# Kernel tuning notes

Measured on AMD Instinct MI355X. Metric: run time of the kernel, lower is better.

## Reference

```python
import jax, jax.numpy as jnp
import numpy as np

EPS = 1e-06


def _feature_map(x):
    # elu(x) + 1  (elu with alpha=1)
    return jnp.where(x > 0, x + 1.0, jnp.exp(x))


def setup_inputs() -> dict:
    key = jax.random.key(0)
    k1, k2, k3 = jax.random.split(key, 3)
    N, L, S, H, D = 4, 8192, 8192, 8, 64
    q = jax.random.normal(k1, (N, L, H, D), dtype=jnp.float32)
    k = jax.random.normal(k2, (N, S, H, D), dtype=jnp.float32)
    v = jax.random.normal(k3, (N, S, H, D), dtype=jnp.float32)
    q_mask = jnp.ones((N, L), dtype=jnp.float32)
    kv_mask = jnp.ones((N, S), dtype=jnp.float32)
    return {"q": q, "k": k, "v": v, "q_mask": q_mask, "kv_mask": kv_mask}


def reference(q, k, v, q_mask, kv_mask):
    # Linear attention with elu+1 feature map (Katharopoulos et al.)
    qf = _feature_map(q)  # [N, L, H, D]
    kf = _feature_map(k)  # [N, S, H, D]
    qf = q_mask[:, :, None, None] * qf
    kf = kv_mask[:, :, None, None] * kf
    vm = kv_mask[:, :, None, None] * v
    S = v.shape[1]
    # global KV state: [N, H, D, Dv]; v scaled by 1/S for numerical stability
    kv = jnp.einsum('nshd,nshv->nhdv', kf, vm / S)
    # normalizer: einsum('nlhd,nshd->nlh') == q . sum_s(k)
    k_sum = kf.sum(axis=1)  # [N, H, D]
    div = 1.0 / (jnp.einsum('nlhd,nhd->nlh', qf, k_sum) + EPS)
    out = S * jnp.einsum('nlhd,nhdv,nlh->nlhv', qf, kv, div)
    return out
```

## Files before the change

kernel.cpp:

```cpp
#include <hip/hip_runtime.h>
#include <math.h>


#define EPS 1e-6f

static constexpr int Nc = 4;
static constexpr int Lc = 8192;
static constexpr int Sc = 8192;
static constexpr int Hc = 8;
static constexpr int NH = Nc * Hc;
static constexpr int STATE = 64 * 64 + 64;
static constexpr int TS = 32;
static constexpr int TSP = 36;
static constexpr int QSP = 68;

typedef __attribute__((ext_vector_type(4))) short short4v;
typedef __attribute__((ext_vector_type(8))) short short8v;
typedef __attribute__((ext_vector_type(4))) float f32x4;

__device__ __forceinline__ float fmap(float x) {
    return x > 0.f ? x + 1.f : __expf(x);
}
__device__ __forceinline__ unsigned short f2bf(float x) {
    unsigned int u = __float_as_uint(x);
    u += 0x7FFFu + ((u >> 16) & 1u);
    return (unsigned short)(u >> 16);
}
__device__ __forceinline__ float bf2f(unsigned short h) {
    return __uint_as_float(((unsigned int)h) << 16);
}
__device__ __forceinline__ short8v ld8(const unsigned short* p) {
    short4v a = *(const short4v*)p;
    short4v b = *(const short4v*)(p + 4);
    return __builtin_shufflevector(a, b, 0, 1, 2, 3, 4, 5, 6, 7);
}
__device__ __forceinline__ unsigned int pack2(unsigned short a, unsigned short b) {
    return (unsigned)a | ((unsigned)b << 16);
}

__global__ __launch_bounds__(256, 4) void k1_partial(
    const float* __restrict__ kg, const float* __restrict__ vg,
    const float* __restrict__ kv_mask,
    float* __restrict__ partial, int chunks, int sc)
{
    __shared__ unsigned short kTh[64][TSP], kTl[64][TSP];
    __shared__ unsigned short vTh[64][TSP], vTl[64][TSP];
    __shared__ float ksb[16][64];

    const int bid = blockIdx.x;
    const int pair = bid / chunks;
    const int chunk = bid - pair * chunks;
    const int n = pair >> 3;
    const int h = pair & 7;
    const int s0 = chunk * sc;
    const int t = threadIdx.x;
    const int g = t >> 4;
    const int c4 = (t & 15) * 4;
    const int lane = t & 63;
    const int wv = t >> 6;
    const int row16 = lane & 15;
    const int g8 = (lane >> 4) * 8;

    f32x4 acc[4] = {{0.f,0.f,0.f,0.f},{0.f,0.f,0.f,0.f},
                    {0.f,0.f,0.f,0.f},{0.f,0.f,0.f,0.f}};
    float ksm[4] = {0.f, 0.f, 0.f, 0.f};

    const size_t rowstride = (size_t)Hc * 64;
    const size_t gbase = ((size_t)n * Sc * Hc + h) * 64 + c4;
    const int mbase = n * Sc;

    float4 kp0, kp1, vp0, vp1;
    float mpe, mpo;

    {
        const int s = s0 + 2 * g;
        const size_t be = gbase + (size_t)s * rowstride;
        kp0 = *(const float4*)(kg + be);
        kp1 = *(const float4*)(kg + be + rowstride);
        vp0 = *(const float4*)(vg + be);
        vp1 = *(const float4*)(vg + be + rowstride);
        mpe = kv_mask[mbase + s];
        mpo = kv_mask[mbase + s + 1];
    }

    for (int sb = 0; sb < sc; sb += TS) {
        const float4 ck0 = kp0, ck1 = kp1, cv0 = vp0, cv1 = vp1;
        const float cme = mpe, cmo = mpo;

        {
            const int nxt = (sb + TS < sc) ? sb + TS : sb;
            const int s = s0 + nxt + 2 * g;
            const size_t be = gbase + (size_t)s * rowstride;
            kp0 = *(const float4*)(kg + be);
            kp1 = *(const float4*)(kg + be + rowstride);
            vp0 = *(const float4*)(vg + be);
            vp1 = *(const float4*)(vg + be + rowstride);
            mpe = kv_mask[mbase + s];
            mpo = kv_mask[mbase + s + 1];
        }

        const float* kep = &ck0.x;
        const float* kop = &ck1.x;
        const float* vep = &cv0.x;
        const float* vop = &cv1.x;
        #pragma unroll
        for (int j = 0; j < 4; ++j) {
            const float fe = cme * fmap(kep[j]);
            const float fo = cmo * fmap(kop[j]);
            ksm[j] += fe + fo;
            const unsigned short he = f2bf(fe), ho = f2bf(fo);
            const unsigned short le = f2bf(fe - bf2f(he)), lo_ = f2bf(fo - bf2f(ho));
            *(unsigned int*)&kTh[c4 + j][2 * g] = pack2(he, ho);
            *(unsigned int*)&kTl[c4 + j][2 * g] = pack2(le, lo_);
            const float ue = cme * vep[j];
            const float uo = cmo * vop[j];
            const unsigned short vhe = f2bf(ue), vho = f2bf(uo);
            const unsigned short vle = f2bf(ue - bf2f(vhe)), vlo = f2bf(uo - bf2f(vho));
            *(unsigned int*)&vTh[c4 + j][2 * g] = pack2(vhe, vho);
            *(unsigned int*)&vTl[c4 + j][2 * g] = pack2(vle, vlo);
        }
        __syncthreads();

        const short8v Ah = ld8(&kTh[wv * 16 + row16][g8]);
        const short8v Al = ld8(&kTl[wv * 16 + row16][g8]);
        #pragma unroll
        for (int bt = 0; bt < 4; ++bt) {
            const short8v Bh = ld8(&vTh[bt * 16 + row16][g8]);
            const short8v Bl = ld8(&vTl[bt * 16 + row16][g8]);
            acc[bt] = __builtin_amdgcn_mfma_f32_16x16x32_bf16(Ah, Bh, acc[bt], 0, 0, 0);
            acc[bt] = __builtin_amdgcn_mfma_f32_16x16x32_bf16(Al, Bh, acc[bt], 0, 0, 0);
            acc[bt] = __builtin_amdgcn_mfma_f32_16x16x32_bf16(Ah, Bl, acc[bt], 0, 0, 0);
        }
        __syncthreads();
    }

    float* outp = partial + (size_t)bid * STATE;
    #pragma unroll
    for (int bt = 0; bt < 4; ++bt) {
        #pragma unroll
        for (int r = 0; r < 4; ++r) {
            outp[(size_t)(wv * 16 + (lane >> 4) * 4 + r) * 64 + bt * 16 + (lane & 15)]
                = acc[bt][r];
        }
    }

    *(f32x4*)&ksb[g][c4] = (f32x4){ksm[0], ksm[1], ksm[2], ksm[3]};
    __syncthreads();
    if (t < 64) {
        float s = 0.f;
        #pragma unroll
        for (int i = 0; i < 16; ++i) s += ksb[i][t];
        outp[4096 + t] = s;
    }
}

__global__ __launch_bounds__(256) void k2_reduce(
    const float* __restrict__ src, float* __restrict__ dst, int nred)
{
    const int p = blockIdx.x / 5;
    const int seg = blockIdx.x - p * 5;
    const int e4 = seg * 256 + threadIdx.x;
    if (e4 >= STATE / 4) return;
    const float4* s = (const float4*)(src + (size_t)p * nred * STATE) + e4;
    float4 acc = make_float4(0.f, 0.f, 0.f, 0.f);
    #pragma unroll 4
    for (int j = 0; j < nred; ++j) {
        float4 x = s[(size_t)j * (STATE / 4)];
        acc.x += x.x; acc.y += x.y; acc.z += x.z; acc.w += x.w;
    }
    ((float4*)(dst + (size_t)p * STATE))[e4] = acc;
}

__global__ __launch_bounds__(256) void k2b_finalize(
    const float* __restrict__ src, float* __restrict__ dst, int nred)
{
    __shared__ float kv[64][QSP];
    __shared__ float kss[64];

    const int pair = blockIdx.x;
    const int t = threadIdx.x;
    const float4* sbase = (const float4*)(src + (size_t)pair * nred * STATE);

    #pragma unroll
    for (int i = 0; i < 4; ++i) {
        const int e4 = t + i * 256;
        float4 a = make_float4(0.f, 0.f, 0.f, 0.f);
        for (int j = 0; j < nred; ++j) {
            float4 x = sbase[(size_t)j * (STATE / 4) + e4];
            a.x += x.x; a.y += x.y; a.z += x.z; a.w += x.w;
        }
        *(float4*)&kv[e4 >> 4][(e4 & 15) * 4] = a;
    }
    if (t < 16) {
        float4 a = make_float4(0.f, 0.f, 0.f, 0.f);
        for (int j = 0; j < nred; ++j) {
            float4 x = sbase[(size_t)j * (STATE / 4) + 1024 + t];
            a.x += x.x; a.y += x.y; a.z += x.z; a.w += x.w;
        }
        *(float4*)&kss[t * 4] = a;
    }
    __syncthreads();

    unsigned int* dw = (unsigned int*)(dst + (size_t)pair * STATE);
    #pragma unroll
    for (int i = 0; i < 8; ++i) {
        const int w = t + i * 256;
        const int dv = w >> 5;
        const int d0 = (w & 31) * 2;
        const float f0 = kv[d0][dv];
        const float f1 = kv[d0 + 1][dv];
        const unsigned short h0 = f2bf(f0), h1 = f2bf(f1);
        dw[w] = pack2(h0, h1);
        dw[2048 + w] = pack2(f2bf(f0 - bf2f(h0)), f2bf(f1 - bf2f(h1)));
    }
    if (t < 64) dst[(size_t)pair * STATE + 4096 + t] = kss[t];
}

__global__ __launch_bounds__(256, 4) void k3_out(
    const float* __restrict__ qg, const float* __restrict__ state,
    const float* __restrict__ q_mask, float* __restrict__ outg)
{
    __shared__ __align__(16) unsigned short qsp[2][64][QSP];
    __shared__ unsigned short kvt[2][64][QSP];
    __shared__ float ksum[64];
    __shared__ float dinv[64];

    const int nblk = Lc / 64;
    const int bid = blockIdx.x;
    const int pair = bid / nblk;
    const int lblk = bid - pair * nblk;
    const int n = pair >> 3;
    const int h = pair & 7;
    const int l0 = lblk * 64;
    const int t = threadIdx.x;
    const int lane = t & 63;
    const int wv = t >> 6;
    const int row16 = lane & 15;
    const int g8 = (lane >> 4) * 8;

    const unsigned int* sw = (const unsigned int*)(state + (size_t)pair * STATE);
    #pragma unroll
    for (int i = 0; i < 8; ++i) {
        const int w = t + i * 256;
        const int dv = w >> 5;
        const int d2 = (w & 31) * 2;
        *(unsigned int*)&kvt[0][dv][d2] = sw[w];
        *(unsigned int*)&kvt[1][dv][d2] = sw[2048 + w];
    }
    if (t < 64) ksum[t] = ((const float*)state)[(size_t)pair * STATE + 4096 + t];
    __syncthreads();

    #pragma unroll
    for (int p = 0; p < 4; ++p) {
        const int f = t + p * 256;
        const int row = f >> 4;
        const int c4 = (f & 15) * 4;
        const int l = l0 + row;
        const size_t base = ((size_t)(n * Lc + l) * Hc + h) * 64 + c4;
        const float4 qq = *(const float4*)(qg + base);
        const float m = q_mask[n * Lc + l];
        const float q0 = m * fmap(qq.x), q1 = m * fmap(qq.y);
        const float q2 = m * fmap(qq.z), q3 = m * fmap(qq.w);
        const unsigned short h0 = f2bf(q0), h1 = f2bf(q1), h2 = f2bf(q2), h3 = f2bf(q3);
        *(unsigned int*)&qsp[0][row][c4]     = pack2(h0, h1);
        *(unsigned int*)&qsp[0][row][c4 + 2] = pack2(h2, h3);
        *(unsigned int*)&qsp[1][row][c4]     = pack2(f2bf(q0 - bf2f(h0)), f2bf(q1 - bf2f(h1)));
        *(unsigned int*)&qsp[1][row][c4 + 2] = pack2(f2bf(q2 - bf2f(h2)), f2bf(q3 - bf2f(h3)));
        float dp = q0 * ksum[c4] + q1 * ksum[c4 + 1] + q2 * ksum[c4 + 2] + q3 * ksum[c4 + 3];
        dp += __shfl_xor(dp, 1);
        dp += __shfl_xor(dp, 2);
        dp += __shfl_xor(dp, 4);
        dp += __shfl_xor(dp, 8);
        if ((t & 15) == 0) dinv[row] = 1.0f / (dp + EPS);
    }
    __syncthreads();

    f32x4 acc[4] = {{0.f,0.f,0.f,0.f},{0.f,0.f,0.f,0.f},
                    {0.f,0.f,0.f,0.f},{0.f,0.f,0.f,0.f}};
    #pragma unroll
    for (int ks = 0; ks < 2; ++ks) {
        const short8v Ah = ld8(&qsp[0][wv * 16 + row16][ks * 32 + g8]);
        const short8v Al = ld8(&qsp[1][wv * 16 + row16][ks * 32 + g8]);
        #pragma unroll
        for (int bt = 0; bt < 4; ++bt) {
            const short8v Bh = ld8(&kvt[0][bt * 16 + row16][ks * 32 + g8]);
            const short8v Bl = ld8(&kvt[1][bt * 16 + row16][ks * 32 + g8]);
            acc[bt] = __builtin_amdgcn_mfma_f32_16x16x32_bf16(Ah, Bh, acc[bt], 0, 0, 0);
            acc[bt] = __builtin_amdgcn_mfma_f32_16x16x32_bf16(Al, Bh, acc[bt], 0, 0, 0);
            acc[bt] = __builtin_amdgcn_mfma_f32_16x16x32_bf16(Ah, Bl, acc[bt], 0, 0, 0);
        }
    }
    __syncthreads();

    float (*outs)[QSP] = reinterpret_cast<float (*)[QSP]>(&qsp[0][0][0]);
    #pragma unroll
    for (int bt = 0; bt < 4; ++bt) {
        #pragma unroll
        for (int r = 0; r < 4; ++r) {
            const int row = wv * 16 + (lane >> 4) * 4 + r;
            outs[row][bt * 16 + row16] = acc[bt][r] * dinv[row];
        }
    }
    __syncthreads();

    #pragma unroll
    for (int p = 0; p < 4; ++p) {
        const int f = t + p * 256;
        const int row = f >> 4;
        const int c4 = (f & 15) * 4;
        const size_t base = ((size_t)(n * Lc + l0 + row) * Hc + h) * 64 + c4;
        *(float4*)(outg + base) = *(const float4*)&outs[row][c4];
    }
}

extern "C" void kernel_launch(void* const* d_in, const int* in_sizes, int n_in,
                              void* d_out, int out_size, void* d_ws, size_t ws_size,
                              hipStream_t stream)
{
    (void)in_sizes; (void)n_in; (void)out_size;
    const float* q       = (const float*)d_in[0];
    const float* k       = (const float*)d_in[1];
    const float* v       = (const float*)d_in[2];
    const float* q_mask  = (const float*)d_in[3];
    const float* kv_mask = (const float*)d_in[4];
    float* out = (float*)d_out;

    const size_t stBytes  = (size_t)STATE * sizeof(float);
    const size_t finBytes = (size_t)NH * stBytes;
    const size_t p2Bytes  = (size_t)NH * 4 * stBytes;

    float* fin = (float*)d_ws;
    float* p2  = (float*)((char*)d_ws + finBytes);
    float* p1  = (float*)((char*)d_ws + finBytes + p2Bytes);

    int chunks = 0;
    for (int c = 64; c >= 8; c >>= 1) {
        if (ws_size >= finBytes + p2Bytes + (size_t)NH * c * stBytes) { chunks = c; break; }
    }

    if (chunks >= 8) {
        k1_partial<<<NH * chunks, 256, 0, stream>>>(k, v, kv_mask, p1, chunks, Sc / chunks);
        k2_reduce<<<NH * 4 * 5, 256, 0, stream>>>(p1, p2, chunks / 4);
        k2b_finalize<<<NH, 256, 0, stream>>>(p2, fin, 4);
    } else {
        float* p1fb = (float*)((char*)d_ws + finBytes);
        k1_partial<<<NH, 256, 0, stream>>>(k, v, kv_mask, p1fb, 1, Sc);
        k2b_finalize<<<NH, 256, 0, stream>>>(p1fb, fin, 1);
    }

    k3_out<<<NH * (Lc / 64), 256, 0, stream>>>(q, fin, q_mask, out);
}
```

Before: 84.81 us.

## Restructure KV-state kernel to single-wave blocks without barriers

The partial KV-state kernel now runs one 64-thread wavefront per block instead of four waves. That single wave loads and converts the whole 32-row tile itself and computes all 16 output tiles of the 64x64 state. This removes the __syncthreads barriers and the shared-memory reduction of the k-sum, which now uses warp shuffles. In exchange, the register-based prefetch of the next tile is dropped, each block has four times as many accumulators and four times the load work, and fewer threads are resident per block. Latency hiding now depends on having many blocks resident at once.

```diff
diff --git a/kernel.cpp b/kernel.cpp
--- a/kernel.cpp
+++ b/kernel.cpp
@@ -38,14 +38,13 @@
     return (unsigned)a | ((unsigned)b << 16);
 }
 
-__global__ __launch_bounds__(256, 4) void k1_partial(
+__global__ __launch_bounds__(64, 2) void k1_partial(
     const float* __restrict__ kg, const float* __restrict__ vg,
     const float* __restrict__ kv_mask,
     float* __restrict__ partial, int chunks, int sc)
 {
     __shared__ unsigned short kTh[64][TSP], kTl[64][TSP];
     __shared__ unsigned short vTh[64][TSP], vTl[64][TSP];
-    __shared__ float ksb[16][64];
 
     const int bid = blockIdx.x;
     const int pair = bid / chunks;
@@ -53,104 +52,88 @@
     const int n = pair >> 3;
     const int h = pair & 7;
     const int s0 = chunk * sc;
-    const int t = threadIdx.x;
-    const int g = t >> 4;
-    const int c4 = (t & 15) * 4;
-    const int lane = t & 63;
-    const int wv = t >> 6;
-    const int row16 = lane & 15;
-    const int g8 = (lane >> 4) * 8;
-
-    f32x4 acc[4] = {{0.f,0.f,0.f,0.f},{0.f,0.f,0.f,0.f},
-                    {0.f,0.f,0.f,0.f},{0.f,0.f,0.f,0.f}};
+    const int l = threadIdx.x;
+    const int row16 = l & 15;
+    const int lg = l >> 4;
+    const int c4 = row16 * 4;
+    const int g8 = lg * 8;
+
+    f32x4 acc[4][4] = {};
     float ksm[4] = {0.f, 0.f, 0.f, 0.f};
 
     const size_t rowstride = (size_t)Hc * 64;
     const size_t gbase = ((size_t)n * Sc * Hc + h) * 64 + c4;
     const int mbase = n * Sc;
 
-    float4 kp0, kp1, vp0, vp1;
-    float mpe, mpo;
-
-    {
-        const int s = s0 + 2 * g;
-        const size_t be = gbase + (size_t)s * rowstride;
-        kp0 = *(const float4*)(kg + be);
-        kp1 = *(const float4*)(kg + be + rowstride);
-        vp0 = *(const float4*)(vg + be);
-        vp1 = *(const float4*)(vg + be + rowstride);
-        mpe = kv_mask[mbase + s];
-        mpo = kv_mask[mbase + s + 1];
-    }
-
     for (int sb = 0; sb < sc; sb += TS) {
-        const float4 ck0 = kp0, ck1 = kp1, cv0 = vp0, cv1 = vp1;
-        const float cme = mpe, cmo = mpo;
-
-        {
-            const int nxt = (sb + TS < sc) ? sb + TS : sb;
-            const int s = s0 + nxt + 2 * g;
+        #pragma unroll
+        for (int jj = 0; jj < 4; ++jj) {
+            const int r0 = jj * 8 + lg * 2;
+            const int s = s0 + sb + r0;
             const size_t be = gbase + (size_t)s * rowstride;
-            kp0 = *(const float4*)(kg + be);
-            kp1 = *(const float4*)(kg + be + rowstride);
-            vp0 = *(const float4*)(vg + be);
-            vp1 = *(const float4*)(vg + be + rowstride);
-            mpe = kv_mask[mbase + s];
-            mpo = kv_mask[mbase + s + 1];
-        }
-
-        const float* kep = &ck0.x;
-        const float* kop = &ck1.x;
-        const float* vep = &cv0.x;
-        const float* vop = &cv1.x;
-        #pragma unroll
-        for (int j = 0; j < 4; ++j) {
-            const float fe = cme * fmap(kep[j]);
-            const float fo = cmo * fmap(kop[j]);
-            ksm[j] += fe + fo;
-            const unsigned short he = f2bf(fe), ho = f2bf(fo);
-            const unsigned short le = f2bf(fe - bf2f(he)), lo_ = f2bf(fo - bf2f(ho));
-            *(unsigned int*)&kTh[c4 + j][2 * g] = pack2(he, ho);
-            *(unsigned int*)&kTl[c4 + j][2 * g] = pack2(le, lo_);
-            const float ue = cme * vep[j];
-            const float uo = cmo * vop[j];
-            const unsigned short vhe = f2bf(ue), vho = f2bf(uo);
-            const unsigned short vle = f2bf(ue - bf2f(vhe)), vlo = f2bf(uo - bf2f(vho));
-            *(unsigned int*)&vTh[c4 + j][2 * g] = pack2(vhe, vho);
-            *(unsigned int*)&vTl[c4 + j][2 * g] = pack2(vle, vlo);
-        }
-        __syncthreads();
-
-        const short8v Ah = ld8(&kTh[wv * 16 + row16][g8]);
-        const short8v Al = ld8(&kTl[wv * 16 + row16][g8]);
+            const float4 k0 = *(const float4*)(kg + be);
+            const float4 k1 = *(const float4*)(kg + be + rowstride);
+            const float4 v0 = *(const float4*)(vg + be);
+            const float4 v1 = *(const float4*)(vg + be + rowstride);
+            const float m0 = kv_mask[mbase + s];
+            const float m1 = kv_mask[mbase + s + 1];
+            const float* ke = &k0.x;
+            const float* ko = &k1.x;
+            const float* ve = &v0.x;
+            const float* vo = &v1.x;
+            #pragma unroll
+            for (int j = 0; j < 4; ++j) {
+                const float fe = m0 * fmap(ke[j]);
+                const float fo = m1 * fmap(ko[j]);
+                ksm[j] += fe + fo;
+                const unsigned short he = f2bf(fe), ho = f2bf(fo);
+                *(unsigned int*)&kTh[c4 + j][r0] = pack2(he, ho);
+                *(unsigned int*)&kTl[c4 + j][r0] =
+                    pack2(f2bf(fe - bf2f(he)), f2bf(fo - bf2f(ho)));
+                const float ue = m0 * ve[j];
+                const float uo = m1 * vo[j];
+                const unsigned short vhe = f2bf(ue), vho = f2bf(uo);
+                *(unsigned int*)&vTh[c4 + j][r0] = pack2(vhe, vho);
+                *(unsigned int*)&vTl[c4 + j][r0] =
+                    pack2(f2bf(ue - bf2f(vhe)), f2bf(uo - bf2f(vho)));
+            }
+        }
+
+        short8v Ah[4], Al[4];
+        #pragma unroll
+        for (int dt = 0; dt < 4; ++dt) {
+            Ah[dt] = ld8(&kTh[dt * 16 + row16][g8]);
+            Al[dt] = ld8(&kTl[dt * 16 + row16][g8]);
+        }
         #pragma unroll
         for (int bt = 0; bt < 4; ++bt) {
             const short8v Bh = ld8(&vTh[bt * 16 + row16][g8]);
             const short8v Bl = ld8(&vTl[bt * 16 + row16][g8]);
-            acc[bt] = __builtin_amdgcn_mfma_f32_16x16x32_bf16(Ah, Bh, acc[bt], 0, 0, 0);
-            acc[bt] = __builtin_amdgcn_mfma_f32_16x16x32_bf16(Al, Bh, acc[bt], 0, 0, 0);
-            acc[bt] = __builtin_amdgcn_mfma_f32_16x16x32_bf16(Ah, Bl, acc[bt], 0, 0, 0);
-        }
-        __syncthreads();
+            #pragma unroll
+            for (int dt = 0; dt < 4; ++dt) {
+                acc[dt][bt] = __builtin_amdgcn_mfma_f32_16x16x32_bf16(Ah[dt], Bh, acc[dt][bt], 0, 0, 0);
+                acc[dt][bt] = __builtin_amdgcn_mfma_f32_16x16x32_bf16(Al[dt], Bh, acc[dt][bt], 0, 0, 0);
+                acc[dt][bt] = __builtin_amdgcn_mfma_f32_16x16x32_bf16(Ah[dt], Bl, acc[dt][bt], 0, 0, 0);
+            }
+        }
     }
 
     float* outp = partial + (size_t)bid * STATE;
     #pragma unroll
-    for (int bt = 0; bt < 4; ++bt) {
-        #pragma unroll
-        for (int r = 0; r < 4; ++r) {
-            outp[(size_t)(wv * 16 + (lane >> 4) * 4 + r) * 64 + bt * 16 + (lane & 15)]
-                = acc[bt][r];
-        }
-    }
-
-    *(f32x4*)&ksb[g][c4] = (f32x4){ksm[0], ksm[1], ksm[2], ksm[3]};
-    __syncthreads();
-    if (t < 64) {
-        float s = 0.f;
-        #pragma unroll
-        for (int i = 0; i < 16; ++i) s += ksb[i][t];
-        outp[4096 + t] = s;
+    for (int dt = 0; dt < 4; ++dt)
+        #pragma unroll
+        for (int bt = 0; bt < 4; ++bt)
+            #pragma unroll
+            for (int r = 0; r < 4; ++r)
+                outp[(size_t)(dt * 16 + lg * 4 + r) * 64 + bt * 16 + row16]
+                    = acc[dt][bt][r];
+
+    #pragma unroll
+    for (int j = 0; j < 4; ++j) {
+        float s = ksm[j];
+        s += __shfl_xor(s, 16);
+        s += __shfl_xor(s, 32);
+        if (lg == 0) outp[4096 + c4 + j] = s;
     }
 }
 
@@ -339,12 +322,12 @@
     }
 
     if (chunks >= 8) {
-        k1_partial<<<NH * chunks, 256, 0, stream>>>(k, v, kv_mask, p1, chunks, Sc / chunks);
+        k1_partial<<<NH * chunks, 64, 0, stream>>>(k, v, kv_mask, p1, chunks, Sc / chunks);
         k2_reduce<<<NH * 4 * 5, 256, 0, stream>>>(p1, p2, chunks / 4);
         k2b_finalize<<<NH, 256, 0, stream>>>(p2, fin, 4);
     } else {
         float* p1fb = (float*)((char*)d_ws + finBytes);
-        k1_partial<<<NH, 256, 0, stream>>>(k, v, kv_mask, p1fb, 1, Sc);
+        k1_partial<<<NH, 64, 0, stream>>>(k, v, kv_mask, p1fb, 1, Sc);
         k2b_finalize<<<NH, 256, 0, stream>>>(p1fb, fin, 1);
     }
 
```

New measurement: 85.83 us. About the same (+1.2%).

## Stream K/V tiles into LDS with async global_load_lds double buffering

Applied to the files above, without the earlier changes.

Replaces the register-based prefetch of K, V and mask with direct global-to-LDS async loads (global_load_lds) into a double-buffered fp32 staging area, then converts from LDS to split-bf16 tiles for MFMA. Manual s_waitcnt and s_barrier calls replace __syncthreads to overlap the next tile's load with the current tile's compute. LDS use grows, so launch bounds drop from 4 to 2 blocks per CU, which lowers occupancy. It also adds an extra LDS round trip per tile.

```diff
diff --git a/kernel.cpp b/kernel.cpp
--- a/kernel.cpp
+++ b/kernel.cpp
@@ -38,14 +38,18 @@
     return (unsigned)a | ((unsigned)b << 16);
 }
 
-__global__ __launch_bounds__(256, 4) void k1_partial(
+__global__ __launch_bounds__(256, 2) void k1_partial(
     const float* __restrict__ kg, const float* __restrict__ vg,
     const float* __restrict__ kv_mask,
     float* __restrict__ partial, int chunks, int sc)
 {
-    __shared__ unsigned short kTh[64][TSP], kTl[64][TSP];
-    __shared__ unsigned short vTh[64][TSP], vTl[64][TSP];
-    __shared__ float ksb[16][64];
+    __shared__ __align__(16) float smemf[8256 + (4 * 64 * TSP) / 2];
+
+    unsigned short* bfb = (unsigned short*)(smemf + 8256);
+    unsigned short* kTh = bfb;
+    unsigned short* kTl = bfb + 64 * TSP;
+    unsigned short* vTh = bfb + 2 * 64 * TSP;
+    unsigned short* vTl = bfb + 3 * 64 * TSP;
 
     const int bid = blockIdx.x;
     const int pair = bid / chunks;
@@ -54,10 +58,10 @@
     const int h = pair & 7;
     const int s0 = chunk * sc;
     const int t = threadIdx.x;
-    const int g = t >> 4;
-    const int c4 = (t & 15) * 4;
     const int lane = t & 63;
     const int wv = t >> 6;
+    const int sg = t >> 4;
+    const int c4 = (t & 15) * 4;
     const int row16 = lane & 15;
     const int g8 = (lane >> 4) * 8;
 
@@ -66,72 +70,88 @@
     float ksm[4] = {0.f, 0.f, 0.f, 0.f};
 
     const size_t rowstride = (size_t)Hc * 64;
-    const size_t gbase = ((size_t)n * Sc * Hc + h) * 64 + c4;
+    const size_t gA = ((size_t)n * Sc * Hc + h) * 64;
     const int mbase = n * Sc;
 
-    float4 kp0, kp1, vp0, vp1;
-    float mpe, mpo;
-
-    {
-        const int s = s0 + 2 * g;
-        const size_t be = gbase + (size_t)s * rowstride;
-        kp0 = *(const float4*)(kg + be);
-        kp1 = *(const float4*)(kg + be + rowstride);
-        vp0 = *(const float4*)(vg + be);
-        vp1 = *(const float4*)(vg + be + rowstride);
-        mpe = kv_mask[mbase + s];
-        mpo = kv_mask[mbase + s + 1];
-    }
-
-    for (int sb = 0; sb < sc; sb += TS) {
-        const float4 ck0 = kp0, ck1 = kp1, cv0 = vp0, cv1 = vp1;
-        const float cme = mpe, cmo = mpo;
+    auto issue = [&](int tt, int nb) {
+        const int sr = s0 + tt * TS;
+        #pragma unroll
+        for (int i = 0; i < 2; ++i) {
+            const int rbase = wv * 8 + i * 4;
+            const int r = rbase + (lane >> 4);
+            const int c = (lane & 15) * 4;
+            const float* gsk = kg + gA + (size_t)(sr + r) * rowstride + c;
+            const float* gsv = vg + gA + (size_t)(sr + r) * rowstride + c;
+            __builtin_amdgcn_global_load_lds(
+                (const __attribute__((address_space(1))) unsigned int*)gsk,
+                (__attribute__((address_space(3))) unsigned int*)&smemf[nb * 2048 + rbase * 64],
+                16, 0, 0);
+            __builtin_amdgcn_global_load_lds(
+                (const __attribute__((address_space(1))) unsigned int*)gsv,
+                (__attribute__((address_space(3))) unsigned int*)&smemf[4096 + nb * 2048 + rbase * 64],
+                16, 0, 0);
+        }
+        if (lane < 8) {
+            const float* gm = kv_mask + mbase + sr + wv * 8 + lane;
+            __builtin_amdgcn_global_load_lds(
+                (const __attribute__((address_space(1))) unsigned int*)gm,
+                (__attribute__((address_space(3))) unsigned int*)&smemf[8192 + nb * 32 + wv * 8],
+                4, 0, 0);
+        }
+    };
+
+    const int NT = sc / TS;
+    issue(0, 0);
+
+    for (int tt = 0; tt < NT; ++tt) {
+        const int nb = tt & 1;
+        const int nxt = (tt + 1 < NT) ? tt + 1 : tt;
+        issue(nxt, nb ^ 1);
+
+        asm volatile("s_waitcnt vmcnt(5)" ::: "memory");
+        __builtin_amdgcn_s_barrier();
 
         {
-            const int nxt = (sb + TS < sc) ? sb + TS : sb;
-            const int s = s0 + nxt + 2 * g;
-            const size_t be = gbase + (size_t)s * rowstride;
-            kp0 = *(const float4*)(kg + be);
-            kp1 = *(const float4*)(kg + be + rowstride);
-            vp0 = *(const float4*)(vg + be);
-            vp1 = *(const float4*)(vg + be + rowstride);
-            mpe = kv_mask[mbase + s];
-            mpo = kv_mask[mbase + s + 1];
-        }
-
-        const float* kep = &ck0.x;
-        const float* kop = &ck1.x;
-        const float* vep = &cv0.x;
-        const float* vop = &cv1.x;
-        #pragma unroll
-        for (int j = 0; j < 4; ++j) {
-            const float fe = cme * fmap(kep[j]);
-            const float fo = cmo * fmap(kop[j]);
-            ksm[j] += fe + fo;
-            const unsigned short he = f2bf(fe), ho = f2bf(fo);
-            const unsigned short le = f2bf(fe - bf2f(he)), lo_ = f2bf(fo - bf2f(ho));
-            *(unsigned int*)&kTh[c4 + j][2 * g] = pack2(he, ho);
-            *(unsigned int*)&kTl[c4 + j][2 * g] = pack2(le, lo_);
-            const float ue = cme * vep[j];
-            const float uo = cmo * vop[j];
-            const unsigned short vhe = f2bf(ue), vho = f2bf(uo);
-            const unsigned short vle = f2bf(ue - bf2f(vhe)), vlo = f2bf(uo - bf2f(vho));
-            *(unsigned int*)&vTh[c4 + j][2 * g] = pack2(vhe, vho);
-            *(unsigned int*)&vTl[c4 + j][2 * g] = pack2(vle, vlo);
-        }
-        __syncthreads();
-
-        const short8v Ah = ld8(&kTh[wv * 16 + row16][g8]);
-        const short8v Al = ld8(&kTl[wv * 16 + row16][g8]);
-        #pragma unroll
-        for (int bt = 0; bt < 4; ++bt) {
-            const short8v Bh = ld8(&vTh[bt * 16 + row16][g8]);
-            const short8v Bl = ld8(&vTl[bt * 16 + row16][g8]);
-            acc[bt] = __builtin_amdgcn_mfma_f32_16x16x32_bf16(Ah, Bh, acc[bt], 0, 0, 0);
-            acc[bt] = __builtin_amdgcn_mfma_f32_16x16x32_bf16(Al, Bh, acc[bt], 0, 0, 0);
-            acc[bt] = __builtin_amdgcn_mfma_f32_16x16x32_bf16(Ah, Bl, acc[bt], 0, 0, 0);
-        }
-        __syncthreads();
+            const float m0 = smemf[8192 + nb * 32 + 2 * sg];
+            const float m1 = smemf[8192 + nb * 32 + 2 * sg + 1];
+            const f32x4 k0 = *(const f32x4*)&smemf[nb * 2048 + (2 * sg) * 64 + c4];
+            const f32x4 k1v = *(const f32x4*)&smemf[nb * 2048 + (2 * sg + 1) * 64 + c4];
+            const f32x4 v0 = *(const f32x4*)&smemf[4096 + nb * 2048 + (2 * sg) * 64 + c4];
+            const f32x4 v1 = *(const f32x4*)&smemf[4096 + nb * 2048 + (2 * sg + 1) * 64 + c4];
+            #pragma unroll
+            for (int j = 0; j < 4; ++j) {
+                const float fe = m0 * fmap(k0[j]);
+                const float fo = m1 * fmap(k1v[j]);
+                ksm[j] += fe + fo;
+                const unsigned short he = f2bf(fe), ho = f2bf(fo);
+                *(unsigned int*)&kTh[(c4 + j) * TSP + 2 * sg] = pack2(he, ho);
+                *(unsigned int*)&kTl[(c4 + j) * TSP + 2 * sg] =
+                    pack2(f2bf(fe - bf2f(he)), f2bf(fo - bf2f(ho)));
+                const float ue = m0 * v0[j];
+                const float uo = m1 * v1[j];
+                const unsigned short vhe = f2bf(ue), vho = f2bf(uo);
+                *(unsigned int*)&vTh[(c4 + j) * TSP + 2 * sg] = pack2(vhe, vho);
+                *(unsigned int*)&vTl[(c4 + j) * TSP + 2 * sg] =
+                    pack2(f2bf(ue - bf2f(vhe)), f2bf(uo - bf2f(vho)));
+            }
+        }
+        asm volatile("s_waitcnt lgkmcnt(0)" ::: "memory");
+        __builtin_amdgcn_s_barrier();
+
+        {
+            const short8v Ah = ld8(&kTh[(wv * 16 + row16) * TSP + g8]);
+            const short8v Al = ld8(&kTl[(wv * 16 + row16) * TSP + g8]);
+            #pragma unroll
+            for (int bt = 0; bt < 4; ++bt) {
+                const short8v Bh = ld8(&vTh[(bt * 16 + row16) * TSP + g8]);
+                const short8v Bl = ld8(&vTl[(bt * 16 + row16) * TSP + g8]);
+                acc[bt] = __builtin_amdgcn_mfma_f32_16x16x32_bf16(Ah, Bh, acc[bt], 0, 0, 0);
+                acc[bt] = __builtin_amdgcn_mfma_f32_16x16x32_bf16(Al, Bh, acc[bt], 0, 0, 0);
+                acc[bt] = __builtin_amdgcn_mfma_f32_16x16x32_bf16(Ah, Bl, acc[bt], 0, 0, 0);
+            }
+        }
+        asm volatile("s_waitcnt lgkmcnt(0)" ::: "memory");
+        __builtin_amdgcn_s_barrier();
     }
 
     float* outp = partial + (size_t)bid * STATE;
@@ -139,17 +159,19 @@
     for (int bt = 0; bt < 4; ++bt) {
         #pragma unroll
         for (int r = 0; r < 4; ++r) {
-            outp[(size_t)(wv * 16 + (lane >> 4) * 4 + r) * 64 + bt * 16 + (lane & 15)]
+            outp[(size_t)(wv * 16 + (lane >> 4) * 4 + r) * 64 + bt * 16 + row16]
                 = acc[bt][r];
         }
     }
 
-    *(f32x4*)&ksb[g][c4] = (f32x4){ksm[0], ksm[1], ksm[2], ksm[3]};
+    __syncthreads();
+    float* ksb = smemf;
+    *(f32x4*)&ksb[sg * 64 + c4] = (f32x4){ksm[0], ksm[1], ksm[2], ksm[3]};
     __syncthreads();
     if (t < 64) {
         float s = 0.f;
         #pragma unroll
-        for (int i = 0; i < 16; ++i) s += ksb[i][t];
+        for (int i = 0; i < 16; ++i) s += ksb[i * 64 + t];
         outp[4096 + t] = s;
     }
 }
```

Result: slower. 87.68 us (+3.4%).

## Double k1 S-tile to 64, drop register prefetch, allow 128 chunks

Applied to the files above, without the earlier changes.

The partial KV-state kernel now stages 64 sequence rows per tile instead of 32. Each thread loads four rows at once instead of prefetching the next tile's two rows into registers, and the MFMA loop runs two k-steps per barrier. The final barrier of the last tile is skipped, and the host may pick up to 128 chunks per head pair when the workspace allows. The aim is fewer barriers and more memory-level parallelism per iteration, at the cost of losing the overlap between loads and compute, doubling LDS use, and possibly a larger reduction pass.

```diff
diff --git a/kernel.cpp b/kernel.cpp
--- a/kernel.cpp
+++ b/kernel.cpp
@@ -10,8 +10,8 @@
 static constexpr int Hc = 8;
 static constexpr int NH = Nc * Hc;
 static constexpr int STATE = 64 * 64 + 64;
-static constexpr int TS = 32;
-static constexpr int TSP = 36;
+static constexpr int TS = 64;
+static constexpr int TSP = 68;
 static constexpr int QSP = 68;
 
 typedef __attribute__((ext_vector_type(4))) short short4v;
@@ -54,10 +54,10 @@
     const int h = pair & 7;
     const int s0 = chunk * sc;
     const int t = threadIdx.x;
-    const int g = t >> 4;
-    const int c4 = (t & 15) * 4;
     const int lane = t & 63;
     const int wv = t >> 6;
+    const int sg = t >> 4;
+    const int c4 = (t & 15) * 4;
     const int row16 = lane & 15;
     const int g8 = (lane >> 4) * 8;
 
@@ -69,69 +69,62 @@
     const size_t gbase = ((size_t)n * Sc * Hc + h) * 64 + c4;
     const int mbase = n * Sc;
 
-    float4 kp0, kp1, vp0, vp1;
-    float mpe, mpo;
-
-    {
-        const int s = s0 + 2 * g;
-        const size_t be = gbase + (size_t)s * rowstride;
-        kp0 = *(const float4*)(kg + be);
-        kp1 = *(const float4*)(kg + be + rowstride);
-        vp0 = *(const float4*)(vg + be);
-        vp1 = *(const float4*)(vg + be + rowstride);
-        mpe = kv_mask[mbase + s];
-        mpo = kv_mask[mbase + s + 1];
-    }
-
-    for (int sb = 0; sb < sc; sb += TS) {
-        const float4 ck0 = kp0, ck1 = kp1, cv0 = vp0, cv1 = vp1;
-        const float cme = mpe, cmo = mpo;
-
-        {
-            const int nxt = (sb + TS < sc) ? sb + TS : sb;
-            const int s = s0 + nxt + 2 * g;
-            const size_t be = gbase + (size_t)s * rowstride;
-            kp0 = *(const float4*)(kg + be);
-            kp1 = *(const float4*)(kg + be + rowstride);
-            vp0 = *(const float4*)(vg + be);
-            vp1 = *(const float4*)(vg + be + rowstride);
-            mpe = kv_mask[mbase + s];
-            mpo = kv_mask[mbase + s + 1];
-        }
-
-        const float* kep = &ck0.x;
-        const float* kop = &ck1.x;
-        const float* vep = &cv0.x;
-        const float* vop = &cv1.x;
-        #pragma unroll
-        for (int j = 0; j < 4; ++j) {
-            const float fe = cme * fmap(kep[j]);
-            const float fo = cmo * fmap(kop[j]);
-            ksm[j] += fe + fo;
-            const unsigned short he = f2bf(fe), ho = f2bf(fo);
-            const unsigned short le = f2bf(fe - bf2f(he)), lo_ = f2bf(fo - bf2f(ho));
-            *(unsigned int*)&kTh[c4 + j][2 * g] = pack2(he, ho);
-            *(unsigned int*)&kTl[c4 + j][2 * g] = pack2(le, lo_);
-            const float ue = cme * vep[j];
-            const float uo = cmo * vop[j];
-            const unsigned short vhe = f2bf(ue), vho = f2bf(uo);
-            const unsigned short vle = f2bf(ue - bf2f(vhe)), vlo = f2bf(uo - bf2f(vho));
-            *(unsigned int*)&vTh[c4 + j][2 * g] = pack2(vhe, vho);
-            *(unsigned int*)&vTl[c4 + j][2 * g] = pack2(vle, vlo);
+    const int NT = sc / TS;
+    for (int tt = 0; tt < NT; ++tt) {
+        const int sr = s0 + tt * TS;
+
+        float4 ka[4], va[4];
+        float m[4];
+        #pragma unroll
+        for (int i = 0; i < 4; ++i) {
+            const int r = 2 * sg + (i & 1) + 32 * (i >> 1);
+            const size_t be = gbase + (size_t)(sr + r) * rowstride;
+            ka[i] = *(const float4*)(kg + be);
+            va[i] = *(const float4*)(vg + be);
+            m[i] = kv_mask[mbase + sr + r];
+        }
+
+        #pragma unroll
+        for (int ph = 0; ph < 2; ++ph) {
+            const float m0 = m[2 * ph], m1 = m[2 * ph + 1];
+            const float* ke = &ka[2 * ph].x;
+            const float* ko = &ka[2 * ph + 1].x;
+            const float* ve = &va[2 * ph].x;
+            const float* vo = &va[2 * ph + 1].x;
+            const int scol = 2 * sg + 32 * ph;
+            #pragma unroll
+            for (int j = 0; j < 4; ++j) {
+                const float fe = m0 * fmap(ke[j]);
+                const float fo = m1 * fmap(ko[j]);
+                ksm[j] += fe + fo;
+                const unsigned short he = f2bf(fe), ho = f2bf(fo);
+                *(unsigned int*)&kTh[c4 + j][scol] = pack2(he, ho);
+                *(unsigned int*)&kTl[c4 + j][scol] =
+                    pack2(f2bf(fe - bf2f(he)), f2bf(fo - bf2f(ho)));
+                const float ue = m0 * ve[j];
+                const float uo = m1 * vo[j];
+                const unsigned short vhe = f2bf(ue), vho = f2bf(uo);
+                *(unsigned int*)&vTh[c4 + j][scol] = pack2(vhe, vho);
+                *(unsigned int*)&vTl[c4 + j][scol] =
+                    pack2(f2bf(ue - bf2f(vhe)), f2bf(uo - bf2f(vho)));
+            }
         }
         __syncthreads();
 
-        const short8v Ah = ld8(&kTh[wv * 16 + row16][g8]);
-        const short8v Al = ld8(&kTl[wv * 16 + row16][g8]);
-        #pragma unroll
-        for (int bt = 0; bt < 4; ++bt) {
-            const short8v Bh = ld8(&vTh[bt * 16 + row16][g8]);
-            const short8v Bl = ld8(&vTl[bt * 16 + row16][g8]);
-            acc[bt] = __builtin_amdgcn_mfma_f32_16x16x32_bf16(Ah, Bh, acc[bt], 0, 0, 0);
-            acc[bt] = __builtin_amdgcn_mfma_f32_16x16x32_bf16(Al, Bh, acc[bt], 0, 0, 0);
-            acc[bt] = __builtin_amdgcn_mfma_f32_16x16x32_bf16(Ah, Bl, acc[bt], 0, 0, 0);
-        }
-        __syncthreads();
+        #pragma unroll
+        for (int ks = 0; ks < 2; ++ks) {
+            const short8v Ah = ld8(&kTh[wv * 16 + row16][32 * ks + g8]);
+            const short8v Al = ld8(&kTl[wv * 16 + row16][32 * ks + g8]);
+            #pragma unroll
+            for (int bt = 0; bt < 4; ++bt) {
+                const short8v Bh = ld8(&vTh[bt * 16 + row16][32 * ks + g8]);
+                const short8v Bl = ld8(&vTl[bt * 16 + row16][32 * ks + g8]);
+                acc[bt] = __builtin_amdgcn_mfma_f32_16x16x32_bf16(Ah, Bh, acc[bt], 0, 0, 0);
+                acc[bt] = __builtin_amdgcn_mfma_f32_16x16x32_bf16(Al, Bh, acc[bt], 0, 0, 0);
+                acc[bt] = __builtin_amdgcn_mfma_f32_16x16x32_bf16(Ah, Bl, acc[bt], 0, 0, 0);
+            }
+        }
+        if (tt + 1 < NT) __syncthreads();
     }
 
     float* outp = partial + (size_t)bid * STATE;
@@ -139,12 +132,12 @@
     for (int bt = 0; bt < 4; ++bt) {
         #pragma unroll
         for (int r = 0; r < 4; ++r) {
-            outp[(size_t)(wv * 16 + (lane >> 4) * 4 + r) * 64 + bt * 16 + (lane & 15)]
+            outp[(size_t)(wv * 16 + (lane >> 4) * 4 + r) * 64 + bt * 16 + row16]
                 = acc[bt][r];
         }
     }
 
-    *(f32x4*)&ksb[g][c4] = (f32x4){ksm[0], ksm[1], ksm[2], ksm[3]};
+    *(f32x4*)&ksb[sg][c4] = (f32x4){ksm[0], ksm[1], ksm[2], ksm[3]};
     __syncthreads();
     if (t < 64) {
         float s = 0.f;
@@ -334,7 +327,7 @@
     float* p1  = (float*)((char*)d_ws + finBytes + p2Bytes);
 
     int chunks = 0;
-    for (int c = 64; c >= 8; c >>= 1) {
+    for (int c = 128; c >= 8; c >>= 1) {
         if (ws_size >= finBytes + p2Bytes + (size_t)NH * c * stBytes) { chunks = c; break; }
     }
 
```

Result: slower. 94.87 us (+11.9%).
